# Kernel tuning notes

Hardware: AMD Instinct MI355X
Metric: run time of the kernel (lower is better)

## Reference

```python
import jax, jax.numpy as jnp
import numpy as np

N_NODES = 100000
N_EDGES = 1600000
D_FEAT = 64
EPS = 1e-07


def setup_inputs() -> dict:
    key = jax.random.key(0)
    k1, k2, k3 = jax.random.split(key, 3)
    x = jax.random.normal(k1, (N_NODES, D_FEAT), dtype=jnp.float32)
    beta = jnp.ones((1,), dtype=jnp.float32)
    edge_row = jnp.sort(jax.random.randint(k2, (N_EDGES,), 0, N_NODES, dtype=jnp.int64))
    edge_col = jax.random.randint(k3, (N_EDGES,), 0, N_NODES, dtype=jnp.int64)
    return {"x": x, "beta": beta, "edge_row": edge_row, "edge_col": edge_col}


def reference(x, beta, edge_row, edge_col):
    # Gather endpoint features: [E, d]
    A = x[edge_row]
    B = x[edge_col]
    # Cosine similarity per edge, scaled by beta: [E]
    inner = jnp.sum(A * B, axis=1)
    norms = jnp.linalg.norm(A, axis=1) * jnp.linalg.norm(B, axis=1)
    sim = beta[0] * (inner / (norms + EPS))
    # Sparse row-wise softmax (tf.sparse.softmax): stable segment softmax over edges grouped by row
    row_max = jax.ops.segment_max(sim, edge_row, num_segments=N_NODES)
    e = jnp.exp(sim - row_max[edge_row])
    row_sum = jax.ops.segment_sum(e, edge_row, num_segments=N_NODES)
    p = e / row_sum[edge_row]  # [E]
    # SPMM: out[i] = sum_{(i,j) in E} p_ij * x[j]
    out = jax.ops.segment_sum(p[:, None] * B, edge_row, num_segments=N_NODES)
    return out
```

## Files before the change

kernel.cpp:

```cpp
#include <hip/hip_runtime.h>
#include <math.h>

#define D_FEAT 64
typedef _Float16 v8h __attribute__((ext_vector_type(8)));
typedef float v4f __attribute__((ext_vector_type(4)));
typedef _Float16 h2 __attribute__((ext_vector_type(2)));

__device__ __forceinline__ v8h u2h8(uint4 u) { v8h v; __builtin_memcpy(&v, &u, 16); return v; }
__device__ __forceinline__ unsigned pkh(float a, float b) {
    h2 r = {(_Float16)a, (_Float16)b};
    unsigned u; __builtin_memcpy(&u, &r, 4); return u;
}

__global__ __launch_bounds__(256)
void agnn_prep(const float* __restrict__ x, float* __restrict__ rn,
               uint2* __restrict__ xh, const int* __restrict__ edge_row,
               int* __restrict__ row_ptr, int n_nodes, int n_edges, int nb_prep) {
    if ((int)blockIdx.x < nb_prep) {
        int t = blockIdx.x * blockDim.x + threadIdx.x;
        int node = t >> 4;
        if (node >= n_nodes) return;
        int l4 = t & 15;
        float4 v = ((const float4*)x)[node * 16 + l4];
        float ss = v.x*v.x + v.y*v.y + v.z*v.z + v.w*v.w;
        #pragma unroll
        for (int off = 1; off < 16; off <<= 1) ss += __shfl_xor(ss, off, 64);
        if (l4 == 0) rn[node] = ss > 0.f ? rsqrtf(ss) : 0.f;
        h2 h0 = {(_Float16)v.x, (_Float16)v.y};
        h2 h1 = {(_Float16)v.z, (_Float16)v.w};
        uint2 u;
        __builtin_memcpy(&u.x, &h0, 4);
        __builtin_memcpy(&u.y, &h1, 4);
        xh[node * 16 + l4] = u;
    } else {
        int e = (blockIdx.x - nb_prep) * blockDim.x + threadIdx.x;
        if (e >= n_edges) return;
        int r1 = edge_row[e];
        int r0 = (e == 0) ? -1 : edge_row[e - 1];
        for (int r = r0 + 1; r <= r1; ++r) row_ptr[r] = e;
        if (e == n_edges - 1)
            for (int r = r1 + 1; r <= n_nodes; ++r) row_ptr[r] = n_edges;
    }
}

#define XCP_PITCH 144
#define WAVE_LDS  (32 * XCP_PITCH)

__global__ __launch_bounds__(128)
void agnn_fused(const float* __restrict__ beta_p,
                const int* __restrict__ edge_col,
                const int* __restrict__ row_ptr,
                const float* __restrict__ rn,
                const uint4* __restrict__ xh4,
                float* __restrict__ out, int n_nodes) {
    __shared__ char lds_raw[2 * WAVE_LDS];
    int wid  = threadIdx.x >> 6;
    int lane = threadIdx.x & 63;
    int q    = lane >> 4;
    int lo4  = lane & 15;
    char* XCP = lds_raw + wid * WAVE_LDS;

    int tile = blockIdx.x;
    int t0 = tile * 16;
    if (t0 >= n_nodes) return;

    int qnode = t0 + lo4; if (qnode >= n_nodes) qnode = n_nodes - 1;
    v8h a0 = u2h8(xh4[(size_t)qnode * 8 + q]);
    v8h a1 = u2h8(xh4[(size_t)qnode * 8 + 4 + q]);

    float beta  = beta_p[0];
    float shift = fabsf(beta);
    float brn = beta * rn[qnode];
    int es   = row_ptr[t0];
    int tend = t0 + 16; if (tend > n_nodes) tend = n_nodes;
    int L    = row_ptr[tend] - es;
    int blo  = row_ptr[min(t0 + lo4,     n_nodes)] - es;
    int bhi  = row_ptr[min(t0 + lo4 + 1, n_nodes)] - es;

    v4f o0 = {0,0,0,0}, o1 = {0,0,0,0}, o2 = {0,0,0,0}, o3 = {0,0,0,0};
    float lsum = 0.f;
    unsigned int selp = (lo4 & 1) ? 0x07060302u : 0x05040100u;
    int srcA = ((q & 1) << 5) + lo4;
    int srcB = srcA + 16;

    int nch  = (L + 31) >> 5;
    int nchw = (nch > wid) ? ((nch - wid + 1) >> 1) : 0;
    if (nchw > 0) {
        int cc0, cc1;
        {
            int i0 = (wid << 5) + lo4, i1 = i0 + 16;
            cc0 = edge_col[es + (i0 < L ? i0 : 0)];
            cc1 = edge_col[es + (i1 < L ? i1 : 0)];
        }
        float rc0 = rn[cc0], rc1 = rn[cc1];
        uint4 A00 = xh4[(size_t)cc0 * 8 + q];
        uint4 A01 = xh4[(size_t)cc0 * 8 + 4 + q];
        uint4 A10 = xh4[(size_t)cc1 * 8 + q];
        uint4 A11 = xh4[(size_t)cc1 * 8 + 4 + q];

        for (int k = 0; k < nchw; ++k) {
            int base = (wid + 2 * k) << 5;
            bool more = (k + 1) < nchw;

            int nc0, nc1;
            if (more) {
                int i0 = base + 64 + lo4, i1 = i0 + 16;
                nc0 = edge_col[es + (i0 < L ? i0 : 0)];
                nc1 = edge_col[es + (i1 < L ? i1 : 0)];
            } else { nc0 = cc0; nc1 = cc1; }

            v4f z0 = {0,0,0,0};
            z0 = __builtin_amdgcn_mfma_f32_16x16x32_f16(u2h8(A00), a0, z0, 0, 0, 0);
            z0 = __builtin_amdgcn_mfma_f32_16x16x32_f16(u2h8(A01), a1, z0, 0, 0, 0);
            v4f z1 = {0,0,0,0};
            z1 = __builtin_amdgcn_mfma_f32_16x16x32_f16(u2h8(A10), a0, z1, 0, 0, 0);
            z1 = __builtin_amdgcn_mfma_f32_16x16x32_f16(u2h8(A11), a1, z1, 0, 0, 0);

            {
                unsigned int colA = lo4 * 4, colB = (16 + lo4) * 4;
                char* pA = XCP + (4 * q) * XCP_PITCH;
                char* pB = XCP + (16 + 4 * q) * XCP_PITCH;
                *(unsigned int*)(pA + 0 * XCP_PITCH + colA) = A00.x;
                *(unsigned int*)(pA + 1 * XCP_PITCH + colA) = A00.y;
                *(unsigned int*)(pA + 2 * XCP_PITCH + colA) = A00.z;
                *(unsigned int*)(pA + 3 * XCP_PITCH + colA) = A00.w;
                *(unsigned int*)(pB + 0 * XCP_PITCH + colA) = A01.x;
                *(unsigned int*)(pB + 1 * XCP_PITCH + colA) = A01.y;
                *(unsigned int*)(pB + 2 * XCP_PITCH + colA) = A01.z;
                *(unsigned int*)(pB + 3 * XCP_PITCH + colA) = A01.w;
                *(unsigned int*)(pA + 0 * XCP_PITCH + colB) = A10.x;
                *(unsigned int*)(pA + 1 * XCP_PITCH + colB) = A10.y;
                *(unsigned int*)(pA + 2 * XCP_PITCH + colB) = A10.z;
                *(unsigned int*)(pA + 3 * XCP_PITCH + colB) = A10.w;
                *(unsigned int*)(pB + 0 * XCP_PITCH + colB) = A11.x;
                *(unsigned int*)(pB + 1 * XCP_PITCH + colB) = A11.y;
                *(unsigned int*)(pB + 2 * XCP_PITCH + colB) = A11.z;
                *(unsigned int*)(pB + 3 * XCP_PITCH + colB) = A11.w;
            }

            float nr0, nr1; uint4 B00, B01, B10, B11;
            if (more) {
                nr0 = rn[nc0]; nr1 = rn[nc1];
                B00 = xh4[(size_t)nc0 * 8 + q];
                B01 = xh4[(size_t)nc0 * 8 + 4 + q];
                B10 = xh4[(size_t)nc1 * 8 + q];
                B11 = xh4[(size_t)nc1 * 8 + 4 + q];
            } else {
                nr0 = rc0; nr1 = rc1;
                B00 = A00; B01 = A01; B10 = A10; B11 = A11;
            }

            float rA0 = __shfl(rc0, 4*q + 0), rA1 = __shfl(rc0, 4*q + 1);
            float rA2 = __shfl(rc0, 4*q + 2), rA3 = __shfl(rc0, 4*q + 3);
            float rB0 = __shfl(rc1, 4*q + 0), rB1 = __shfl(rc1, 4*q + 1);
            float rB2 = __shfl(rc1, 4*q + 2), rB3 = __shfl(rc1, 4*q + 3);

            int eA = base + 4 * q, eB = eA + 16;
            float wA0 = (eA+0 >= blo && eA+0 < bhi) ? __expf(brn * rA0 * z0[0] - shift) : 0.f;
            float wA1 = (eA+1 >= blo && eA+1 < bhi) ? __expf(brn * rA1 * z0[1] - shift) : 0.f;
            float wA2 = (eA+2 >= blo && eA+2 < bhi) ? __expf(brn * rA2 * z0[2] - shift) : 0.f;
            float wA3 = (eA+3 >= blo && eA+3 < bhi) ? __expf(brn * rA3 * z0[3] - shift) : 0.f;
            float wB0 = (eB+0 >= blo && eB+0 < bhi) ? __expf(brn * rB0 * z1[0] - shift) : 0.f;
            float wB1 = (eB+1 >= blo && eB+1 < bhi) ? __expf(brn * rB1 * z1[1] - shift) : 0.f;
            float wB2 = (eB+2 >= blo && eB+2 < bhi) ? __expf(brn * rB2 * z1[2] - shift) : 0.f;
            float wB3 = (eB+3 >= blo && eB+3 < bhi) ? __expf(brn * rB3 * z1[3] - shift) : 0.f;
            lsum += ((wA0 + wA1) + (wA2 + wA3)) + ((wB0 + wB1) + (wB2 + wB3));

            unsigned d0 = pkh(wA0, wA1), d1 = pkh(wA2, wA3);
            unsigned e0 = pkh(wB0, wB1), e1 = pkh(wB2, wB3);
            unsigned uA0 = __shfl((int)d0, srcA), uA1 = __shfl((int)d1, srcA);
            unsigned uB0 = __shfl((int)d0, srcB), uB1 = __shfl((int)d1, srcB);
            unsigned vA0 = __shfl((int)e0, srcA), vA1 = __shfl((int)e1, srcA);
            unsigned vB0 = __shfl((int)e0, srcB), vB1 = __shfl((int)e1, srcB);
            uint4 pu;
            if (q < 2) { pu.x = uA0; pu.y = uA1; pu.z = uB0; pu.w = uB1; }
            else       { pu.x = vA0; pu.y = vA1; pu.z = vB0; pu.w = vB1; }
            v8h pah = u2h8(pu);

            {
                const char* rp = XCP + (0 + (lo4 >> 1)) * XCP_PITCH + q * 32;
                uint4 da = *(const uint4*)rp;
                uint4 db = *(const uint4*)(rp + 16);
                uint4 bb = { __builtin_amdgcn_perm(da.y, da.x, selp),
                             __builtin_amdgcn_perm(da.w, da.z, selp),
                             __builtin_amdgcn_perm(db.y, db.x, selp),
                             __builtin_amdgcn_perm(db.w, db.z, selp) };
                o0 = __builtin_amdgcn_mfma_f32_16x16x32_f16(pah, u2h8(bb), o0, 0, 0, 0);
            }
            {
                const char* rp = XCP + (8 + (lo4 >> 1)) * XCP_PITCH + q * 32;
                uint4 da = *(const uint4*)rp;
                uint4 db = *(const uint4*)(rp + 16);
                uint4 bb = { __builtin_amdgcn_perm(da.y, da.x, selp),
                             __builtin_amdgcn_perm(da.w, da.z, selp),
                             __builtin_amdgcn_perm(db.y, db.x, selp),
                             __builtin_amdgcn_perm(db.w, db.z, selp) };
                o1 = __builtin_amdgcn_mfma_f32_16x16x32_f16(pah, u2h8(bb), o1, 0, 0, 0);
            }
            {
                const char* rp = XCP + (16 + (lo4 >> 1)) * XCP_PITCH + q * 32;
                uint4 da = *(const uint4*)rp;
                uint4 db = *(const uint4*)(rp + 16);
                uint4 bb = { __builtin_amdgcn_perm(da.y, da.x, selp),
                             __builtin_amdgcn_perm(da.w, da.z, selp),
                             __builtin_amdgcn_perm(db.y, db.x, selp),
                             __builtin_amdgcn_perm(db.w, db.z, selp) };
                o2 = __builtin_amdgcn_mfma_f32_16x16x32_f16(pah, u2h8(bb), o2, 0, 0, 0);
            }
            {
                const char* rp = XCP + (24 + (lo4 >> 1)) * XCP_PITCH + q * 32;
                uint4 da = *(const uint4*)rp;
                uint4 db = *(const uint4*)(rp + 16);
                uint4 bb = { __builtin_amdgcn_perm(da.y, da.x, selp),
                             __builtin_amdgcn_perm(da.w, da.z, selp),
                             __builtin_amdgcn_perm(db.y, db.x, selp),
                             __builtin_amdgcn_perm(db.w, db.z, selp) };
                o3 = __builtin_amdgcn_mfma_f32_16x16x32_f16(pah, u2h8(bb), o3, 0, 0, 0);
            }

            cc0 = nc0; cc1 = nc1; rc0 = nr0; rc1 = nr1;
            A00 = B00; A01 = B01; A10 = B10; A11 = B11;
        }
    }

    if (wid == 1) {
        char* ST = XCP;
        *(v4f*)(ST + lane * 68 +  0) = o0;
        *(v4f*)(ST + lane * 68 + 16) = o1;
        *(v4f*)(ST + lane * 68 + 32) = o2;
        *(v4f*)(ST + lane * 68 + 48) = o3;
        *(float*)(ST + 64 * 68 + lane * 4) = lsum;
    }
    __syncthreads();
    if (wid == 1) return;
    {
        const char* ST = lds_raw + WAVE_LDS;
        o0 += *(const v4f*)(ST + lane * 68 +  0);
        o1 += *(const v4f*)(ST + lane * 68 + 16);
        o2 += *(const v4f*)(ST + lane * 68 + 32);
        o3 += *(const v4f*)(ST + lane * 68 + 48);
        lsum += *(const float*)(ST + 64 * 68 + lane * 4);
    }

    lsum += __shfl_xor(lsum, 16, 64);
    lsum += __shfl_xor(lsum, 32, 64);
    float inv = lsum > 0.f ? 1.f / lsum : 0.f;
    float i0 = __shfl(inv, 4*q + 0);
    float i1 = __shfl(inv, 4*q + 1);
    float i2 = __shfl(inv, 4*q + 2);
    float i3 = __shfl(inv, 4*q + 3);

    int m0 = t0 + q * 4;
    if (m0 + 0 < n_nodes) { float* p = out + (size_t)(m0 + 0) * 64 + lo4;
        p[0] = o0[0]*i0; p[16] = o1[0]*i0; p[32] = o2[0]*i0; p[48] = o3[0]*i0; }
    if (m0 + 1 < n_nodes) { float* p = out + (size_t)(m0 + 1) * 64 + lo4;
        p[0] = o0[1]*i1; p[16] = o1[1]*i1; p[32] = o2[1]*i1; p[48] = o3[1]*i1; }
    if (m0 + 2 < n_nodes) { float* p = out + (size_t)(m0 + 2) * 64 + lo4;
        p[0] = o0[2]*i2; p[16] = o1[2]*i2; p[32] = o2[2]*i2; p[48] = o3[2]*i2; }
    if (m0 + 3 < n_nodes) { float* p = out + (size_t)(m0 + 3) * 64 + lo4;
        p[0] = o0[3]*i3; p[16] = o1[3]*i3; p[32] = o2[3]*i3; p[48] = o3[3]*i3; }
}

extern "C" void kernel_launch(void* const* d_in, const int* in_sizes, int n_in,
                              void* d_out, int out_size, void* d_ws, size_t ws_size,
                              hipStream_t stream) {
    const float* x        = (const float*)d_in[0];
    const float* beta     = (const float*)d_in[1];
    const int*   edge_row = (const int*)d_in[2];
    const int*   edge_col = (const int*)d_in[3];
    float* out = (float*)d_out;

    int n_nodes = in_sizes[0] / D_FEAT;
    int n_edges = in_sizes[2];

    char* ws = (char*)d_ws;
    float* rn = (float*)ws;
    size_t off0 = ((size_t)n_nodes * sizeof(float) + 255) & ~(size_t)255;
    int* row_ptr = (int*)(ws + off0);
    size_t off1 = off0 + (((size_t)(n_nodes + 1) * sizeof(int) + 255) & ~(size_t)255);
    uint2* xh = (uint2*)(ws + off1);

    {
        int nb_prep = (n_nodes * 16 + 255) / 256;
        int nb_rp   = (n_edges + 255) / 256;
        agnn_prep<<<nb_prep + nb_rp, 256, 0, stream>>>(
            x, rn, xh, edge_row, row_ptr, n_nodes, n_edges, nb_prep);
    }
    {
        int tiles = (n_nodes + 15) / 16;
        agnn_fused<<<tiles, 128, 0, stream>>>(beta, edge_col, row_ptr,
                                              rn, (const uint4*)xh, out, n_nodes);
    }
}
```

Baseline: 126.3 us.

## Merge prep and fused kernels into one cooperative persistent kernel with grid sync

Combines the preprocessing pass (norms, fp16 conversion, row_ptr build) and the fused attention/SpMM pass into one cooperative kernel. A grid-wide sync separates the two phases, and the second phase loops over tiles persistently. This removes a kernel launch and the gap between the two kernels. In exchange it caps the grid at the occupancy limit, adds the cost of a grid barrier, and loses the load balancing that a full-size tile grid gave the hardware scheduler. The old two-kernel path stays as a fallback if the cooperative launch fails.

```diff
diff --git a/kernel.cpp b/kernel.cpp
--- a/kernel.cpp
+++ b/kernel.cpp
@@ -1,5 +1,8 @@
 #include <hip/hip_runtime.h>
+#include <hip/hip_cooperative_groups.h>
 #include <math.h>
+
+namespace cg = cooperative_groups;
 
 #define D_FEAT 64
 typedef _Float16 v8h __attribute__((ext_vector_type(8)));
@@ -10,6 +13,256 @@
 __device__ __forceinline__ unsigned pkh(float a, float b) {
     h2 r = {(_Float16)a, (_Float16)b};
     unsigned u; __builtin_memcpy(&u, &r, 4); return u;
+}
+
+#define XCP_PITCH 144
+#define WAVE_LDS  (32 * XCP_PITCH)
+
+__global__ __launch_bounds__(128)
+void agnn_mega(const float* __restrict__ x, const float* __restrict__ beta_p,
+               const int* __restrict__ edge_row, const int* __restrict__ edge_col,
+               float* __restrict__ rn, int* __restrict__ row_ptr,
+               uint2* __restrict__ xh, float* __restrict__ out,
+               int n_nodes, int n_edges) {
+    __shared__ char lds_raw[2 * WAVE_LDS];
+    const uint4* xh4 = (const uint4*)xh;
+    int gsize = gridDim.x * blockDim.x;
+    int gtid  = blockIdx.x * blockDim.x + threadIdx.x;
+
+    int nwork = n_nodes * 16;
+    for (int t = gtid; t < nwork; t += gsize) {
+        int node = t >> 4;
+        int l4   = t & 15;
+        float4 v = ((const float4*)x)[t];
+        float ss = v.x*v.x + v.y*v.y + v.z*v.z + v.w*v.w;
+        #pragma unroll
+        for (int off = 1; off < 16; off <<= 1) ss += __shfl_xor(ss, off, 64);
+        if (l4 == 0) rn[node] = ss > 0.f ? rsqrtf(ss) : 0.f;
+        h2 h0 = {(_Float16)v.x, (_Float16)v.y};
+        h2 h1 = {(_Float16)v.z, (_Float16)v.w};
+        uint2 u;
+        __builtin_memcpy(&u.x, &h0, 4);
+        __builtin_memcpy(&u.y, &h1, 4);
+        xh[t] = u;
+    }
+    for (int e = gtid; e < n_edges; e += gsize) {
+        int r1 = edge_row[e];
+        int r0 = (e == 0) ? -1 : edge_row[e - 1];
+        for (int r = r0 + 1; r <= r1; ++r) row_ptr[r] = e;
+        if (e == n_edges - 1)
+            for (int r = r1 + 1; r <= n_nodes; ++r) row_ptr[r] = n_edges;
+    }
+
+    cg::this_grid().sync();
+
+    int wid  = threadIdx.x >> 6;
+    int lane = threadIdx.x & 63;
+    int q    = lane >> 4;
+    int lo4  = lane & 15;
+    char* XCP = lds_raw + wid * WAVE_LDS;
+
+    float beta  = beta_p[0];
+    float shift = fabsf(beta);
+    unsigned int selp = (lo4 & 1) ? 0x07060302u : 0x05040100u;
+    int srcA = ((q & 1) << 5) + lo4;
+    int srcB = srcA + 16;
+    int tiles = (n_nodes + 15) >> 4;
+
+    for (int tile = blockIdx.x; tile < tiles; tile += gridDim.x) {
+        int t0 = tile * 16;
+
+        int qnode = t0 + lo4; if (qnode >= n_nodes) qnode = n_nodes - 1;
+        v8h a0 = u2h8(xh4[(size_t)qnode * 8 + q]);
+        v8h a1 = u2h8(xh4[(size_t)qnode * 8 + 4 + q]);
+
+        int rb = t0 + q * 4;
+        float brn = beta * rn[qnode];
+        int es   = row_ptr[t0];
+        int tend = t0 + 16; if (tend > n_nodes) tend = n_nodes;
+        int L    = row_ptr[tend] - es;
+        int blo  = row_ptr[min(t0 + lo4,     n_nodes)] - es;
+        int bhi  = row_ptr[min(t0 + lo4 + 1, n_nodes)] - es;
+
+        v4f o0 = {0,0,0,0}, o1 = {0,0,0,0}, o2 = {0,0,0,0}, o3 = {0,0,0,0};
+        float lsum = 0.f;
+
+        int nch  = (L + 31) >> 5;
+        int nchw = (nch > wid) ? ((nch - wid + 1) >> 1) : 0;
+        if (nchw > 0) {
+            int cc0, cc1;
+            {
+                int i0 = (wid << 5) + lo4, i1 = i0 + 16;
+                cc0 = edge_col[es + (i0 < L ? i0 : 0)];
+                cc1 = edge_col[es + (i1 < L ? i1 : 0)];
+            }
+            float rc0 = rn[cc0], rc1 = rn[cc1];
+            uint4 A00 = xh4[(size_t)cc0 * 8 + q];
+            uint4 A01 = xh4[(size_t)cc0 * 8 + 4 + q];
+            uint4 A10 = xh4[(size_t)cc1 * 8 + q];
+            uint4 A11 = xh4[(size_t)cc1 * 8 + 4 + q];
+
+            for (int k = 0; k < nchw; ++k) {
+                int base = (wid + 2 * k) << 5;
+                bool more = (k + 1) < nchw;
+
+                int nc0, nc1;
+                if (more) {
+                    int i0 = base + 64 + lo4, i1 = i0 + 16;
+                    nc0 = edge_col[es + (i0 < L ? i0 : 0)];
+                    nc1 = edge_col[es + (i1 < L ? i1 : 0)];
+                } else { nc0 = cc0; nc1 = cc1; }
+
+                v4f z0 = {0,0,0,0};
+                z0 = __builtin_amdgcn_mfma_f32_16x16x32_f16(u2h8(A00), a0, z0, 0, 0, 0);
+                z0 = __builtin_amdgcn_mfma_f32_16x16x32_f16(u2h8(A01), a1, z0, 0, 0, 0);
+                v4f z1 = {0,0,0,0};
+                z1 = __builtin_amdgcn_mfma_f32_16x16x32_f16(u2h8(A10), a0, z1, 0, 0, 0);
+                z1 = __builtin_amdgcn_mfma_f32_16x16x32_f16(u2h8(A11), a1, z1, 0, 0, 0);
+
+                {
+                    unsigned int colA = lo4 * 4, colB = (16 + lo4) * 4;
+                    char* pA = XCP + (4 * q) * XCP_PITCH;
+                    char* pB = XCP + (16 + 4 * q) * XCP_PITCH;
+                    *(unsigned int*)(pA + 0 * XCP_PITCH + colA) = A00.x;
+                    *(unsigned int*)(pA + 1 * XCP_PITCH + colA) = A00.y;
+                    *(unsigned int*)(pA + 2 * XCP_PITCH + colA) = A00.z;
+                    *(unsigned int*)(pA + 3 * XCP_PITCH + colA) = A00.w;
+                    *(unsigned int*)(pB + 0 * XCP_PITCH + colA) = A01.x;
+                    *(unsigned int*)(pB + 1 * XCP_PITCH + colA) = A01.y;
+                    *(unsigned int*)(pB + 2 * XCP_PITCH + colA) = A01.z;
+                    *(unsigned int*)(pB + 3 * XCP_PITCH + colA) = A01.w;
+                    *(unsigned int*)(pA + 0 * XCP_PITCH + colB) = A10.x;
+                    *(unsigned int*)(pA + 1 * XCP_PITCH + colB) = A10.y;
+                    *(unsigned int*)(pA + 2 * XCP_PITCH + colB) = A10.z;
+                    *(unsigned int*)(pA + 3 * XCP_PITCH + colB) = A10.w;
+                    *(unsigned int*)(pB + 0 * XCP_PITCH + colB) = A11.x;
+                    *(unsigned int*)(pB + 1 * XCP_PITCH + colB) = A11.y;
+                    *(unsigned int*)(pB + 2 * XCP_PITCH + colB) = A11.z;
+                    *(unsigned int*)(pB + 3 * XCP_PITCH + colB) = A11.w;
+                }
+
+                float nr0, nr1; uint4 B00, B01, B10, B11;
+                if (more) {
+                    nr0 = rn[nc0]; nr1 = rn[nc1];
+                    B00 = xh4[(size_t)nc0 * 8 + q];
+                    B01 = xh4[(size_t)nc0 * 8 + 4 + q];
+                    B10 = xh4[(size_t)nc1 * 8 + q];
+                    B11 = xh4[(size_t)nc1 * 8 + 4 + q];
+                } else {
+                    nr0 = rc0; nr1 = rc1;
+                    B00 = A00; B01 = A01; B10 = A10; B11 = A11;
+                }
+
+                float rA0 = __shfl(rc0, 4*q + 0), rA1 = __shfl(rc0, 4*q + 1);
+                float rA2 = __shfl(rc0, 4*q + 2), rA3 = __shfl(rc0, 4*q + 3);
+                float rB0 = __shfl(rc1, 4*q + 0), rB1 = __shfl(rc1, 4*q + 1);
+                float rB2 = __shfl(rc1, 4*q + 2), rB3 = __shfl(rc1, 4*q + 3);
+
+                int eA = base + 4 * q, eB = eA + 16;
+                float wA0 = (eA+0 >= blo && eA+0 < bhi) ? __expf(brn * rA0 * z0[0] - shift) : 0.f;
+                float wA1 = (eA+1 >= blo && eA+1 < bhi) ? __expf(brn * rA1 * z0[1] - shift) : 0.f;
+                float wA2 = (eA+2 >= blo && eA+2 < bhi) ? __expf(brn * rA2 * z0[2] - shift) : 0.f;
+                float wA3 = (eA+3 >= blo && eA+3 < bhi) ? __expf(brn * rA3 * z0[3] - shift) : 0.f;
+                float wB0 = (eB+0 >= blo && eB+0 < bhi) ? __expf(brn * rB0 * z1[0] - shift) : 0.f;
+                float wB1 = (eB+1 >= blo && eB+1 < bhi) ? __expf(brn * rB1 * z1[1] - shift) : 0.f;
+                float wB2 = (eB+2 >= blo && eB+2 < bhi) ? __expf(brn * rB2 * z1[2] - shift) : 0.f;
+                float wB3 = (eB+3 >= blo && eB+3 < bhi) ? __expf(brn * rB3 * z1[3] - shift) : 0.f;
+                lsum += ((wA0 + wA1) + (wA2 + wA3)) + ((wB0 + wB1) + (wB2 + wB3));
+
+                unsigned d0 = pkh(wA0, wA1), d1 = pkh(wA2, wA3);
+                unsigned e0 = pkh(wB0, wB1), e1 = pkh(wB2, wB3);
+                unsigned uA0 = __shfl((int)d0, srcA), uA1 = __shfl((int)d1, srcA);
+                unsigned uB0 = __shfl((int)d0, srcB), uB1 = __shfl((int)d1, srcB);
+                unsigned vA0 = __shfl((int)e0, srcA), vA1 = __shfl((int)e1, srcA);
+                unsigned vB0 = __shfl((int)e0, srcB), vB1 = __shfl((int)e1, srcB);
+                uint4 pu;
+                if (q < 2) { pu.x = uA0; pu.y = uA1; pu.z = uB0; pu.w = uB1; }
+                else       { pu.x = vA0; pu.y = vA1; pu.z = vB0; pu.w = vB1; }
+                v8h pah = u2h8(pu);
+
+                {
+                    const char* rp = XCP + (0 + (lo4 >> 1)) * XCP_PITCH + q * 32;
+                    uint4 da = *(const uint4*)rp;
+                    uint4 db = *(const uint4*)(rp + 16);
+                    uint4 bb = { __builtin_amdgcn_perm(da.y, da.x, selp),
+                                 __builtin_amdgcn_perm(da.w, da.z, selp),
+                                 __builtin_amdgcn_perm(db.y, db.x, selp),
+                                 __builtin_amdgcn_perm(db.w, db.z, selp) };
+                    o0 = __builtin_amdgcn_mfma_f32_16x16x32_f16(pah, u2h8(bb), o0, 0, 0, 0);
+                }
+                {
+                    const char* rp = XCP + (8 + (lo4 >> 1)) * XCP_PITCH + q * 32;
+                    uint4 da = *(const uint4*)rp;
+                    uint4 db = *(const uint4*)(rp + 16);
+                    uint4 bb = { __builtin_amdgcn_perm(da.y, da.x, selp),
+                                 __builtin_amdgcn_perm(da.w, da.z, selp),
+                                 __builtin_amdgcn_perm(db.y, db.x, selp),
+                                 __builtin_amdgcn_perm(db.w, db.z, selp) };
+                    o1 = __builtin_amdgcn_mfma_f32_16x16x32_f16(pah, u2h8(bb), o1, 0, 0, 0);
+                }
+                {
+                    const char* rp = XCP + (16 + (lo4 >> 1)) * XCP_PITCH + q * 32;
+                    uint4 da = *(const uint4*)rp;
+                    uint4 db = *(const uint4*)(rp + 16);
+                    uint4 bb = { __builtin_amdgcn_perm(da.y, da.x, selp),
+                                 __builtin_amdgcn_perm(da.w, da.z, selp),
+                                 __builtin_amdgcn_perm(db.y, db.x, selp),
+                                 __builtin_amdgcn_perm(db.w, db.z, selp) };
+                    o2 = __builtin_amdgcn_mfma_f32_16x16x32_f16(pah, u2h8(bb), o2, 0, 0, 0);
+                }
+                {
+                    const char* rp = XCP + (24 + (lo4 >> 1)) * XCP_PITCH + q * 32;
+                    uint4 da = *(const uint4*)rp;
+                    uint4 db = *(const uint4*)(rp + 16);
+                    uint4 bb = { __builtin_amdgcn_perm(da.y, da.x, selp),
+                                 __builtin_amdgcn_perm(da.w, da.z, selp),
+                                 __builtin_amdgcn_perm(db.y, db.x, selp),
+                                 __builtin_amdgcn_perm(db.w, db.z, selp) };
+                    o3 = __builtin_amdgcn_mfma_f32_16x16x32_f16(pah, u2h8(bb), o3, 0, 0, 0);
+                }
+
+                cc0 = nc0; cc1 = nc1; rc0 = nr0; rc1 = nr1;
+                A00 = B00; A01 = B01; A10 = B10; A11 = B11;
+            }
+        }
+
+        if (wid == 1) {
+            char* ST = XCP;
+            *(v4f*)(ST + lane * 68 +  0) = o0;
+            *(v4f*)(ST + lane * 68 + 16) = o1;
+            *(v4f*)(ST + lane * 68 + 32) = o2;
+            *(v4f*)(ST + lane * 68 + 48) = o3;
+            *(float*)(ST + 64 * 68 + lane * 4) = lsum;
+        }
+        __syncthreads();
+        if (wid == 0) {
+            const char* ST = lds_raw + WAVE_LDS;
+            o0 += *(const v4f*)(ST + lane * 68 +  0);
+            o1 += *(const v4f*)(ST + lane * 68 + 16);
+            o2 += *(const v4f*)(ST + lane * 68 + 32);
+            o3 += *(const v4f*)(ST + lane * 68 + 48);
+            lsum += *(const float*)(ST + 64 * 68 + lane * 4);
+
+            lsum += __shfl_xor(lsum, 16, 64);
+            lsum += __shfl_xor(lsum, 32, 64);
+            float inv = lsum > 0.f ? 1.f / lsum : 0.f;
+            float i0 = __shfl(inv, 4*q + 0);
+            float i1 = __shfl(inv, 4*q + 1);
+            float i2 = __shfl(inv, 4*q + 2);
+            float i3 = __shfl(inv, 4*q + 3);
+
+            int m0 = rb;
+            if (m0 + 0 < n_nodes) { float* p = out + (size_t)(m0 + 0) * 64 + lo4;
+                p[0] = o0[0]*i0; p[16] = o1[0]*i0; p[32] = o2[0]*i0; p[48] = o3[0]*i0; }
+            if (m0 + 1 < n_nodes) { float* p = out + (size_t)(m0 + 1) * 64 + lo4;
+                p[0] = o0[1]*i1; p[16] = o1[1]*i1; p[32] = o2[1]*i1; p[48] = o3[1]*i1; }
+            if (m0 + 2 < n_nodes) { float* p = out + (size_t)(m0 + 2) * 64 + lo4;
+                p[0] = o0[2]*i2; p[16] = o1[2]*i2; p[32] = o2[2]*i2; p[48] = o3[2]*i2; }
+            if (m0 + 3 < n_nodes) { float* p = out + (size_t)(m0 + 3) * 64 + lo4;
+                p[0] = o0[3]*i3; p[16] = o1[3]*i3; p[32] = o2[3]*i3; p[48] = o3[3]*i3; }
+        }
+        __syncthreads();
+    }
 }
 
 __global__ __launch_bounds__(256)
@@ -43,9 +296,6 @@
     }
 }
 
-#define XCP_PITCH 144
-#define WAVE_LDS  (32 * XCP_PITCH)
-
 __global__ __launch_bounds__(128)
 void agnn_fused(const float* __restrict__ beta_p,
                 const int* __restrict__ edge_col,
@@ -280,14 +530,34 @@
     size_t off1 = off0 + (((size_t)(n_nodes + 1) * sizeof(int) + 255) & ~(size_t)255);
     uint2* xh = (uint2*)(ws + off1);
 
+    static int coop_grid = -1;
+    if (coop_grid < 0) {
+        int dev = 0; hipGetDevice(&dev);
+        int sup = 0;
+        hipDeviceGetAttribute(&sup, hipDeviceAttributeCooperativeLaunch, dev);
+        int maxb = 0, ncu = 0;
+        hipOccupancyMaxActiveBlocksPerMultiprocessor(&maxb, agnn_mega, 128, 0);
+        hipDeviceGetAttribute(&ncu, hipDeviceAttributeMultiprocessorCount, dev);
+        coop_grid = (sup && maxb > 0 && ncu > 0) ? maxb * ncu : 0;
+    }
+
+    int tiles = (n_nodes + 15) / 16;
+    if (coop_grid > 0) {
+        int grid = coop_grid < tiles ? coop_grid : tiles;
+        void* args[] = {(void*)&x, (void*)&beta, (void*)&edge_row, (void*)&edge_col,
+                        (void*)&rn, (void*)&row_ptr, (void*)&xh, (void*)&out,
+                        (void*)&n_nodes, (void*)&n_edges};
+        hipError_t err = hipLaunchCooperativeKernel((void*)agnn_mega, dim3(grid),
+                                                    dim3(128), args, 0, stream);
+        if (err == hipSuccess) return;
+        coop_grid = 0;
+    }
+
     {
         int nb_prep = (n_nodes * 16 + 255) / 256;
         int nb_rp   = (n_edges + 255) / 256;
         agnn_prep<<<nb_prep + nb_rp, 256, 0, stream>>>(
             x, rn, xh, edge_row, row_ptr, n_nodes, n_edges, nb_prep);
-    }
-    {
-        int tiles = (n_nodes + 15) / 16;
         agnn_fused<<<tiles, 128, 0, stream>>>(beta, edge_col, row_ptr,
                                               rn, (const uint4*)xh, out, n_nodes);
     }
```

Result: slower. 233.2 us (+84.7%).

## Quantize node features to per-row int8 to halve gather bandwidth

Applied to the files above, without the earlier changes.

Prep now stores each node's features as offset-biased uint8 with a per-row scale, packed alongside the reciprocal norm as two halfs. The fused kernel gathers 64 bytes per neighbor instead of 128, then dequantizes to fp16 with a perm-and-subtract trick before the MFMAs. The row scale is folded into the edge weight so the SpMM accumulates on integer-valued fp16. This targets the random-gather memory traffic, at the cost of extra ALU work for dequantization and reduced precision (int8 features, fp16 scale and norm).

```diff
diff --git a/kernel.cpp b/kernel.cpp
--- a/kernel.cpp
+++ b/kernel.cpp
@@ -11,27 +11,52 @@
     h2 r = {(_Float16)a, (_Float16)b};
     unsigned u; __builtin_memcpy(&u, &r, 4); return u;
 }
+__device__ __forceinline__ uint4 dq8(uint2 d) {
+    unsigned t0 = __builtin_amdgcn_perm(0u, d.x, 0x04010400u) + 0x65006500u;
+    unsigned t1 = __builtin_amdgcn_perm(0u, d.x, 0x04030402u) + 0x65006500u;
+    unsigned t2 = __builtin_amdgcn_perm(0u, d.y, 0x04010400u) + 0x65006500u;
+    unsigned t3 = __builtin_amdgcn_perm(0u, d.y, 0x04030402u) + 0x65006500u;
+    uint4 u = {t0, t1, t2, t3};
+    v8h h = u2h8(u);
+    const _Float16 c = (_Float16)1408.f;
+    v8h o = {c, c, c, c, c, c, c, c};
+    h = h - o;
+    uint4 r; __builtin_memcpy(&r, &h, 16); return r;
+}
+__device__ __forceinline__ float2 uph(unsigned u) {
+    h2 h; __builtin_memcpy(&h, &u, 4);
+    return make_float2((float)h[0], (float)h[1]);
+}
 
 __global__ __launch_bounds__(256)
-void agnn_prep(const float* __restrict__ x, float* __restrict__ rn,
-               uint2* __restrict__ xh, const int* __restrict__ edge_row,
+void agnn_prep(const float* __restrict__ x, unsigned* __restrict__ rnt,
+               unsigned* __restrict__ xq, const int* __restrict__ edge_row,
                int* __restrict__ row_ptr, int n_nodes, int n_edges, int nb_prep) {
     if ((int)blockIdx.x < nb_prep) {
         int t = blockIdx.x * blockDim.x + threadIdx.x;
         int node = t >> 4;
         if (node >= n_nodes) return;
         int l4 = t & 15;
-        float4 v = ((const float4*)x)[node * 16 + l4];
+        float4 v = ((const float4*)x)[t];
         float ss = v.x*v.x + v.y*v.y + v.z*v.z + v.w*v.w;
+        float am = fmaxf(fmaxf(fabsf(v.x), fabsf(v.y)), fmaxf(fabsf(v.z), fabsf(v.w)));
         #pragma unroll
-        for (int off = 1; off < 16; off <<= 1) ss += __shfl_xor(ss, off, 64);
-        if (l4 == 0) rn[node] = ss > 0.f ? rsqrtf(ss) : 0.f;
-        h2 h0 = {(_Float16)v.x, (_Float16)v.y};
-        h2 h1 = {(_Float16)v.z, (_Float16)v.w};
-        uint2 u;
-        __builtin_memcpy(&u.x, &h0, 4);
-        __builtin_memcpy(&u.y, &h1, 4);
-        xh[node * 16 + l4] = u;
+        for (int off = 1; off < 16; off <<= 1) {
+            ss += __shfl_xor(ss, off, 64);
+            am = fmaxf(am, __shfl_xor(am, off, 64));
+        }
+        float inv_s = am > 0.f ? 127.f / am : 0.f;
+        unsigned b0 = (unsigned)(int)rintf(v.x * inv_s) + 128u;
+        unsigned b1 = (unsigned)(int)rintf(v.y * inv_s) + 128u;
+        unsigned b2 = (unsigned)(int)rintf(v.z * inv_s) + 128u;
+        unsigned b3 = (unsigned)(int)rintf(v.w * inv_s) + 128u;
+        xq[t] = b0 | (b1 << 8) | (b2 << 16) | (b3 << 24);
+        if (l4 == 0) {
+            float s = am * (1.f / 127.f);
+            float nrm = sqrtf(ss);
+            float rnp = nrm > 0.f ? s / nrm : 0.f;
+            rnt[node] = pkh(rnp, s);
+        }
     } else {
         int e = (blockIdx.x - nb_prep) * blockDim.x + threadIdx.x;
         if (e >= n_edges) return;
@@ -50,8 +75,8 @@
 void agnn_fused(const float* __restrict__ beta_p,
                 const int* __restrict__ edge_col,
                 const int* __restrict__ row_ptr,
-                const float* __restrict__ rn,
-                const uint4* __restrict__ xh4,
+                const unsigned* __restrict__ rnt,
+                const uint2* __restrict__ x8,
                 float* __restrict__ out, int n_nodes) {
     __shared__ char lds_raw[2 * WAVE_LDS];
     int wid  = threadIdx.x >> 6;
@@ -65,12 +90,15 @@
     if (t0 >= n_nodes) return;
 
     int qnode = t0 + lo4; if (qnode >= n_nodes) qnode = n_nodes - 1;
-    v8h a0 = u2h8(xh4[(size_t)qnode * 8 + q]);
-    v8h a1 = u2h8(xh4[(size_t)qnode * 8 + 4 + q]);
+    uint2 qL = x8[(size_t)qnode * 8 + q];
+    uint2 qH = x8[(size_t)qnode * 8 + 4 + q];
+    v8h a0 = u2h8(dq8(qL));
+    v8h a1 = u2h8(dq8(qH));
 
     float beta  = beta_p[0];
     float shift = fabsf(beta);
-    float brn = beta * rn[qnode];
+    float2 rq = uph(rnt[qnode]);
+    float brn = beta * rq.x;
     int es   = row_ptr[t0];
     int tend = t0 + 16; if (tend > n_nodes) tend = n_nodes;
     int L    = row_ptr[tend] - es;
@@ -92,11 +120,11 @@
             cc0 = edge_col[es + (i0 < L ? i0 : 0)];
             cc1 = edge_col[es + (i1 < L ? i1 : 0)];
         }
-        float rc0 = rn[cc0], rc1 = rn[cc1];
-        uint4 A00 = xh4[(size_t)cc0 * 8 + q];
-        uint4 A01 = xh4[(size_t)cc0 * 8 + 4 + q];
-        uint4 A10 = xh4[(size_t)cc1 * 8 + q];
-        uint4 A11 = xh4[(size_t)cc1 * 8 + 4 + q];
+        unsigned rcu0 = rnt[cc0], rcu1 = rnt[cc1];
+        uint2 L0 = x8[(size_t)cc0 * 8 + q];
+        uint2 H0 = x8[(size_t)cc0 * 8 + 4 + q];
+        uint2 L1 = x8[(size_t)cc1 * 8 + q];
+        uint2 H1 = x8[(size_t)cc1 * 8 + 4 + q];
 
         for (int k = 0; k < nchw; ++k) {
             int base = (wid + 2 * k) << 5;
@@ -108,6 +136,8 @@
                 nc0 = edge_col[es + (i0 < L ? i0 : 0)];
                 nc1 = edge_col[es + (i1 < L ? i1 : 0)];
             } else { nc0 = cc0; nc1 = cc1; }
+
+            uint4 A00 = dq8(L0), A01 = dq8(H0), A10 = dq8(L1), A11 = dq8(H1);
 
             v4f z0 = {0,0,0,0};
             z0 = __builtin_amdgcn_mfma_f32_16x16x32_f16(u2h8(A00), a0, z0, 0, 0, 0);
@@ -138,36 +168,42 @@
                 *(unsigned int*)(pB + 3 * XCP_PITCH + colB) = A11.w;
             }
 
-            float nr0, nr1; uint4 B00, B01, B10, B11;
+            unsigned nru0, nru1; uint2 NL0, NH0, NL1, NH1;
             if (more) {
-                nr0 = rn[nc0]; nr1 = rn[nc1];
-                B00 = xh4[(size_t)nc0 * 8 + q];
-                B01 = xh4[(size_t)nc0 * 8 + 4 + q];
-                B10 = xh4[(size_t)nc1 * 8 + q];
-                B11 = xh4[(size_t)nc1 * 8 + 4 + q];
+                nru0 = rnt[nc0]; nru1 = rnt[nc1];
+                NL0 = x8[(size_t)nc0 * 8 + q];
+                NH0 = x8[(size_t)nc0 * 8 + 4 + q];
+                NL1 = x8[(size_t)nc1 * 8 + q];
+                NH1 = x8[(size_t)nc1 * 8 + 4 + q];
             } else {
-                nr0 = rc0; nr1 = rc1;
-                B00 = A00; B01 = A01; B10 = A10; B11 = A11;
-            }
-
-            float rA0 = __shfl(rc0, 4*q + 0), rA1 = __shfl(rc0, 4*q + 1);
-            float rA2 = __shfl(rc0, 4*q + 2), rA3 = __shfl(rc0, 4*q + 3);
-            float rB0 = __shfl(rc1, 4*q + 0), rB1 = __shfl(rc1, 4*q + 1);
-            float rB2 = __shfl(rc1, 4*q + 2), rB3 = __shfl(rc1, 4*q + 3);
+                nru0 = rcu0; nru1 = rcu1;
+                NL0 = L0; NH0 = H0; NL1 = L1; NH1 = H1;
+            }
+
+            float2 RA0 = uph(__shfl((int)rcu0, 4*q + 0));
+            float2 RA1 = uph(__shfl((int)rcu0, 4*q + 1));
+            float2 RA2 = uph(__shfl((int)rcu0, 4*q + 2));
+            float2 RA3 = uph(__shfl((int)rcu0, 4*q + 3));
+            float2 RB0 = uph(__shfl((int)rcu1, 4*q + 0));
+            float2 RB1 = uph(__shfl((int)rcu1, 4*q + 1));
+            float2 RB2 = uph(__shfl((int)rcu1, 4*q + 2));
+            float2 RB3 = uph(__shfl((int)rcu1, 4*q + 3));
 
             int eA = base + 4 * q, eB = eA + 16;
-            float wA0 = (eA+0 >= blo && eA+0 < bhi) ? __expf(brn * rA0 * z0[0] - shift) : 0.f;
-            float wA1 = (eA+1 >= blo && eA+1 < bhi) ? __expf(brn * rA1 * z0[1] - shift) : 0.f;
-            float wA2 = (eA+2 >= blo && eA+2 < bhi) ? __expf(brn * rA2 * z0[2] - shift) : 0.f;
-            float wA3 = (eA+3 >= blo && eA+3 < bhi) ? __expf(brn * rA3 * z0[3] - shift) : 0.f;
-            float wB0 = (eB+0 >= blo && eB+0 < bhi) ? __expf(brn * rB0 * z1[0] - shift) : 0.f;
-            float wB1 = (eB+1 >= blo && eB+1 < bhi) ? __expf(brn * rB1 * z1[1] - shift) : 0.f;
-            float wB2 = (eB+2 >= blo && eB+2 < bhi) ? __expf(brn * rB2 * z1[2] - shift) : 0.f;
-            float wB3 = (eB+3 >= blo && eB+3 < bhi) ? __expf(brn * rB3 * z1[3] - shift) : 0.f;
+            float wA0 = (eA+0 >= blo && eA+0 < bhi) ? __expf(brn * RA0.x * z0[0] - shift) : 0.f;
+            float wA1 = (eA+1 >= blo && eA+1 < bhi) ? __expf(brn * RA1.x * z0[1] - shift) : 0.f;
+            float wA2 = (eA+2 >= blo && eA+2 < bhi) ? __expf(brn * RA2.x * z0[2] - shift) : 0.f;
+            float wA3 = (eA+3 >= blo && eA+3 < bhi) ? __expf(brn * RA3.x * z0[3] - shift) : 0.f;
+            float wB0 = (eB+0 >= blo && eB+0 < bhi) ? __expf(brn * RB0.x * z1[0] - shift) : 0.f;
+            float wB1 = (eB+1 >= blo && eB+1 < bhi) ? __expf(brn * RB1.x * z1[1] - shift) : 0.f;
+            float wB2 = (eB+2 >= blo && eB+2 < bhi) ? __expf(brn * RB2.x * z1[2] - shift) : 0.f;
+            float wB3 = (eB+3 >= blo && eB+3 < bhi) ? __expf(brn * RB3.x * z1[3] - shift) : 0.f;
             lsum += ((wA0 + wA1) + (wA2 + wA3)) + ((wB0 + wB1) + (wB2 + wB3));
 
-            unsigned d0 = pkh(wA0, wA1), d1 = pkh(wA2, wA3);
-            unsigned e0 = pkh(wB0, wB1), e1 = pkh(wB2, wB3);
+            unsigned d0 = pkh(wA0 * RA0.y, wA1 * RA1.y);
+            unsigned d1 = pkh(wA2 * RA2.y, wA3 * RA3.y);
+            unsigned e0 = pkh(wB0 * RB0.y, wB1 * RB1.y);
+            unsigned e1 = pkh(wB2 * RB2.y, wB3 * RB3.y);
             unsigned uA0 = __shfl((int)d0, srcA), uA1 = __shfl((int)d1, srcA);
             unsigned uB0 = __shfl((int)d0, srcB), uB1 = __shfl((int)d1, srcB);
             unsigned vA0 = __shfl((int)e0, srcA), vA1 = __shfl((int)e1, srcA);
@@ -218,8 +254,8 @@
                 o3 = __builtin_amdgcn_mfma_f32_16x16x32_f16(pah, u2h8(bb), o3, 0, 0, 0);
             }
 
-            cc0 = nc0; cc1 = nc1; rc0 = nr0; rc1 = nr1;
-            A00 = B00; A01 = B01; A10 = B10; A11 = B11;
+            cc0 = nc0; cc1 = nc1; rcu0 = nru0; rcu1 = nru1;
+            L0 = NL0; H0 = NH0; L1 = NL1; H1 = NH1;
         }
     }
 
@@ -274,21 +310,21 @@
     int n_edges = in_sizes[2];
 
     char* ws = (char*)d_ws;
-    float* rn = (float*)ws;
-    size_t off0 = ((size_t)n_nodes * sizeof(float) + 255) & ~(size_t)255;
+    unsigned* rnt = (unsigned*)ws;
+    size_t off0 = ((size_t)n_nodes * 4 + 255) & ~(size_t)255;
     int* row_ptr = (int*)(ws + off0);
-    size_t off1 = off0 + (((size_t)(n_nodes + 1) * sizeof(int) + 255) & ~(size_t)255);
-    uint2* xh = (uint2*)(ws + off1);
+    size_t off1 = off0 + (((size_t)(n_nodes + 1) * 4 + 255) & ~(size_t)255);
+    unsigned* xq = (unsigned*)(ws + off1);
 
     {
         int nb_prep = (n_nodes * 16 + 255) / 256;
         int nb_rp   = (n_edges + 255) / 256;
         agnn_prep<<<nb_prep + nb_rp, 256, 0, stream>>>(
-            x, rn, xh, edge_row, row_ptr, n_nodes, n_edges, nb_prep);
+            x, rnt, xq, edge_row, row_ptr, n_nodes, n_edges, nb_prep);
     }
     {
         int tiles = (n_nodes + 15) / 16;
         agnn_fused<<<tiles, 128, 0, stream>>>(beta, edge_col, row_ptr,
-                                              rn, (const uint4*)xh, out, n_nodes);
-    }
-}
+                                              rnt, (const uint2*)xq, out, n_nodes);
+    }
+}
```

New measurement: 125.2 us. Within noise of the previous version (-0.9%).
